# Kernel optimization log

Measured on AMD Instinct MI355X. Metric: run time of the kernel, lower is better.

## Reference

```python
import jax, jax.numpy as jnp
import numpy as np

IN_F, OUT_F, NUM_GRIDS, BATCH = 2048, 2048, 8, 4096


def setup_inputs() -> dict:
    key = jax.random.key(0)
    ks = jax.random.split(key, 5)
    x = jax.random.normal(ks[0], (BATCH, IN_F), dtype=jnp.float32)
    # kaiming_uniform_(a=sqrt(5)) on Linear weight -> U(-b, b), b = 1/sqrt(in_features)
    bound = 1.0 / np.sqrt(IN_F)
    base_w = jax.random.uniform(ks[1], (OUT_F, IN_F), dtype=jnp.float32, minval=-bound, maxval=bound)
    base_b = jnp.zeros((OUT_F,), dtype=jnp.float32)
    spline_weight = 0.1 * jax.random.normal(ks[2], (OUT_F, IN_F, NUM_GRIDS), dtype=jnp.float32)
    grid = jnp.linspace(-2.0, 2.0, NUM_GRIDS, dtype=jnp.float32)
    adaptive_gate = jnp.ones((OUT_F,), dtype=jnp.float32)
    feature_importance = jnp.ones((IN_F,), dtype=jnp.float32)
    return {"x": x, "base_w": base_w, "base_b": base_b,
            "spline_weight": spline_weight, "grid": grid,
            "adaptive_gate": adaptive_gate, "feature_importance": feature_importance}


def reference(x, base_w, base_b, spline_weight, grid, adaptive_gate, feature_importance):
    # feature gating
    x_weighted = x * jax.nn.sigmoid(feature_importance)[None, :]          # [b, i]
    # base path: Linear
    base_output = x_weighted @ base_w.T + base_b                          # [b, o]
    # spline path: RBF basis over grid
    x_norm = jnp.tanh(x_weighted)                                         # [b, i]
    basis = jnp.exp(-((x_norm[:, :, None] - grid[None, None, :]) ** 2) * 2.0)  # [b, i, g]
    # F.normalize(p=1, dim=-1): divide by L1 norm clamped to eps
    denom = jnp.maximum(jnp.sum(jnp.abs(basis), axis=-1, keepdims=True), 1e-12)
    basis = basis / denom
    spline_output = jnp.einsum('big,oig->bo', basis, spline_weight)       # [b, o]
    gate = jax.nn.sigmoid(adaptive_gate)[None, :]                         # [1, o]
    return gate * spline_output + (1.0 - gate) * base_output
```

## Files before the change

### kernel.cpp

```cpp
#include <hip/hip_runtime.h>
#include <hip/hip_bf16.h>

#define IN_F   2048
#define OUT_F  2048
#define NG     8
#define BATCH  4096
#define KDIM   (IN_F * (NG + 1))
#define BK     64
#define NT     (KDIM / BK)
#define BM     256
#define BN     128
#define ASZ    (BM * BK * 2)
#define BSZ    (BN * BK * 2)
#define BUFSZ  (ASZ + BSZ)

typedef short bf16x8 __attribute__((ext_vector_type(8)));
typedef float f32x4  __attribute__((ext_vector_type(4)));
typedef __attribute__((address_space(3))) unsigned char       lds_u8;
typedef const __attribute__((address_space(1))) unsigned char glb_u8;

__device__ __forceinline__ float sigmoidf_(float v) {
    return 1.0f / (1.0f + __expf(-v));
}

__device__ __forceinline__ unsigned short f2bf(float f) {
    unsigned int u = __builtin_bit_cast(unsigned int, f);
    u = (u + 0x7fffu + ((u >> 16) & 1u)) >> 16;
    return (unsigned short)u;
}

__global__ __launch_bounds__(256) void act_kernel(
    const float* __restrict__ x, const float* __restrict__ fi,
    const float* __restrict__ gr, unsigned short* __restrict__ Abf)
{
    const int base = blockIdx.x * 1024;
    const int tid  = threadIdx.x;
    const int b    = base >> 11;
    const float4 g0 = *(const float4*)gr;
    const float4 g1 = *(const float4*)(gr + 4);
    unsigned short* rowp = Abf + (size_t)b * KDIM;

#pragma unroll
    for (int e = 0; e < 4; ++e) {
        const int idx = base + tid + e * 256;
        const int i   = idx & (IN_F - 1);
        const float s  = sigmoidf_(fi[i]);
        const float xw = x[idx] * s;
        const float ex = __expf(2.0f * xw);
        const float xn = (ex - 1.0f) / (ex + 1.0f);

        float ev[NG];
        float d;
        d = xn - g0.x; ev[0] = __expf(-2.0f * d * d);
        d = xn - g0.y; ev[1] = __expf(-2.0f * d * d);
        d = xn - g0.z; ev[2] = __expf(-2.0f * d * d);
        d = xn - g0.w; ev[3] = __expf(-2.0f * d * d);
        d = xn - g1.x; ev[4] = __expf(-2.0f * d * d);
        d = xn - g1.y; ev[5] = __expf(-2.0f * d * d);
        d = xn - g1.z; ev[6] = __expf(-2.0f * d * d);
        d = xn - g1.w; ev[7] = __expf(-2.0f * d * d);
        float denom = ((ev[0] + ev[1]) + (ev[2] + ev[3])) +
                      ((ev[4] + ev[5]) + (ev[6] + ev[7]));
        const float rinv = 1.0f / fmaxf(denom, 1e-12f);

        union { unsigned short us[8]; int4 v; } pk;
#pragma unroll
        for (int g = 0; g < NG; ++g) pk.us[g] = f2bf(ev[g] * rinv);
        *(int4*)(rowp + i * NG) = pk.v;
        rowp[IN_F * NG + i] = f2bf(xw);
    }
}

__global__ __launch_bounds__(256) void wprep_kernel(
    const float* __restrict__ bw, const float* __restrict__ sw,
    const float* __restrict__ ag, unsigned short* __restrict__ Wbf)
{
    const int base = blockIdx.x * 1024;
    const int tid  = threadIdx.x;
    const int o    = base >> 11;
    const float gate = sigmoidf_(ag[o]);
    const float og   = 1.0f - gate;
    unsigned short* rowp = Wbf + (size_t)o * KDIM;

#pragma unroll
    for (int e = 0; e < 4; ++e) {
        const int idx = base + tid + e * 256;
        const int i   = idx & (IN_F - 1);
        const float4 s0 = *(const float4*)(sw + (size_t)idx * NG);
        const float4 s1 = *(const float4*)(sw + (size_t)idx * NG + 4);
        union { unsigned short us[8]; int4 v; } pk;
        pk.us[0] = f2bf(gate * s0.x); pk.us[1] = f2bf(gate * s0.y);
        pk.us[2] = f2bf(gate * s0.z); pk.us[3] = f2bf(gate * s0.w);
        pk.us[4] = f2bf(gate * s1.x); pk.us[5] = f2bf(gate * s1.y);
        pk.us[6] = f2bf(gate * s1.z); pk.us[7] = f2bf(gate * s1.w);
        *(int4*)(rowp + i * NG) = pk.v;
        rowp[IN_F * NG + i] = f2bf(og * bw[idx]);
    }
}

#define MFMA(d, a, b) d = __builtin_amdgcn_mfma_f32_16x16x32_bf16(a, b, d, 0, 0, 0)

#define LDA(m) (*(const bf16x8*)(lds + curBase + oA##m))
#define LDB(n) (*(const bf16x8*)(lds + curBase + oB##n))

#define GLA(j) __builtin_amdgcn_global_load_lds((glb_u8*)(aS##j + ko), \
                   (lds_u8*)(lds + stBase + aO##j), 16, 0, 0)
#define GLB(j) __builtin_amdgcn_global_load_lds((glb_u8*)(bS##j + ko), \
                   (lds_u8*)(lds + stBase + bO##j), 16, 0, 0)

__global__ __launch_bounds__(512, 2) void gemm_kernel(
    const unsigned short* __restrict__ A, const unsigned short* __restrict__ B,
    const float* __restrict__ bb, const float* __restrict__ ag,
    float* __restrict__ C)
{
    __shared__ __align__(16) unsigned char lds[3 * BUFSZ];

    const int tid = threadIdx.x;
    const int bid = blockIdx.x;
    const int swz = ((bid & 7) << 5) + (bid >> 3);
    const int bm = swz >> 4, bn = swz & 15;

    const int lane = tid & 63, wid = tid >> 6;
    const int ks = wid & 1, wn = (wid >> 1) & 1, wm = wid >> 2;
    const int fr = lane & 15, kg = lane >> 4;
    const int kq = 4 * ks + kg;

#define MKSA(j)                                                         \
    const int eA##j = tid + (j) * 512;                                  \
    const int rA_##j = eA##j >> 3, cA_##j = (eA##j & 7) ^ (rA_##j & 7); \
    const unsigned short* aS##j = A + (size_t)(bm * BM + rA_##j) * KDIM + cA_##j * 8; \
    const int aO##j = eA##j * 16;
    MKSA(0) MKSA(1) MKSA(2) MKSA(3)
#define MKSB(j)                                                         \
    const int eB##j = tid + (j) * 512;                                  \
    const int rB_##j = eB##j >> 3, cB_##j = (eB##j & 7) ^ (rB_##j & 7); \
    const unsigned short* bS##j = B + (size_t)(bn * BN + rB_##j) * KDIM + cB_##j * 8; \
    const int bO##j = ASZ + eB##j * 16;
    MKSB(0) MKSB(1)

#define MKOA(m)                                                \
    const int rAm##m = wm * 128 + (m) * 16 + fr;               \
    const int oA##m = rAm##m * 128 + ((kq ^ (rAm##m & 7)) << 4);
    MKOA(0) MKOA(1) MKOA(2) MKOA(3) MKOA(4) MKOA(5) MKOA(6) MKOA(7)
#define MKOB(n)                                                \
    const int rBn##n = wn * 64 + (n) * 16 + fr;                \
    const int oB##n = ASZ + rBn##n * 128 + ((kq ^ (rBn##n & 7)) << 4);
    MKOB(0) MKOB(1) MKOB(2) MKOB(3)

    f32x4 acc[8][4] = {};

    {
        const int stBase = 0; const long ko = 0;
        GLA(0); GLA(1); GLA(2); GLA(3); GLB(0); GLB(1);
    }
    {
        const int stBase = BUFSZ; const long ko = BK;
        GLA(0); GLA(1); GLA(2); GLA(3); GLB(0); GLB(1);
    }
    asm volatile("s_waitcnt vmcnt(6)" ::: "memory");
    __builtin_amdgcn_s_barrier();
    __builtin_amdgcn_sched_barrier(0);

    int curBase = 0;
    for (int t = 0; t < NT; ++t) {
        const int stBase = (curBase >= BUFSZ) ? (curBase - BUFSZ)
                                              : (curBase + 2 * BUFSZ);
        const bool doSt = (t + 2) < NT;
        const long ko = (long)(t + 2) * BK;

        bf16x8 vb0 = LDB(0), vb1 = LDB(1), vb2 = LDB(2), vb3 = LDB(3);
        bf16x8 va0 = LDA(0), va1 = LDA(1), va2 = LDA(2), va3 = LDA(3);
        bf16x8 va4 = LDA(4), va5 = LDA(5), va6 = LDA(6), va7 = LDA(7);
        if (doSt) { GLA(0); GLA(1); GLA(2); GLA(3); GLB(0); GLB(1); }

        __builtin_amdgcn_s_setprio(1);
        MFMA(acc[0][0], va0, vb0); MFMA(acc[0][1], va0, vb1);
        MFMA(acc[0][2], va0, vb2); MFMA(acc[0][3], va0, vb3);
        MFMA(acc[1][0], va1, vb0); MFMA(acc[1][1], va1, vb1);
        MFMA(acc[1][2], va1, vb2); MFMA(acc[1][3], va1, vb3);
        MFMA(acc[2][0], va2, vb0); MFMA(acc[2][1], va2, vb1);
        MFMA(acc[2][2], va2, vb2); MFMA(acc[2][3], va2, vb3);
        MFMA(acc[3][0], va3, vb0); MFMA(acc[3][1], va3, vb1);
        MFMA(acc[3][2], va3, vb2); MFMA(acc[3][3], va3, vb3);
        MFMA(acc[4][0], va4, vb0); MFMA(acc[4][1], va4, vb1);
        MFMA(acc[4][2], va4, vb2); MFMA(acc[4][3], va4, vb3);
        MFMA(acc[5][0], va5, vb0); MFMA(acc[5][1], va5, vb1);
        MFMA(acc[5][2], va5, vb2); MFMA(acc[5][3], va5, vb3);
        MFMA(acc[6][0], va6, vb0); MFMA(acc[6][1], va6, vb1);
        MFMA(acc[6][2], va6, vb2); MFMA(acc[6][3], va6, vb3);
        MFMA(acc[7][0], va7, vb0); MFMA(acc[7][1], va7, vb1);
        MFMA(acc[7][2], va7, vb2); MFMA(acc[7][3], va7, vb3);
        __builtin_amdgcn_s_setprio(0);

        __builtin_amdgcn_sched_barrier(0);
        if (doSt) { asm volatile("s_waitcnt vmcnt(6)" ::: "memory"); }
        else      { asm volatile("s_waitcnt vmcnt(0)" ::: "memory"); }
        __builtin_amdgcn_s_barrier();
        __builtin_amdgcn_sched_barrier(0);

        curBase = (curBase == 2 * BUFSZ) ? 0 : (curBase + BUFSZ);
    }

    const int slot = wm * 2 + wn;
    if (ks == 1) {
#pragma unroll
        for (int m = 0; m < 8; ++m)
#pragma unroll
            for (int n = 0; n < 4; ++n)
                *(f32x4*)(lds + slot * 32768 + (m * 4 + n) * 1024 + lane * 16)
                    = acc[m][n];
    }
    __syncthreads();
    if (ks == 0) {
        const int colb = bn * BN + wn * 64;
        const int rowb = bm * BM + wm * 128;
#pragma unroll
        for (int n = 0; n < 4; ++n) {
            const int col = colb + n * 16 + fr;
            const float gate = sigmoidf_(ag[col]);
            const float bias = (1.0f - gate) * bb[col];
#pragma unroll
            for (int m = 0; m < 8; ++m) {
                const f32x4 part =
                    *(const f32x4*)(lds + slot * 32768 + (m * 4 + n) * 1024 + lane * 16);
                const int r0 = rowb + m * 16 + kg * 4;
#pragma unroll
                for (int j = 0; j < 4; ++j)
                    C[(size_t)(r0 + j) * OUT_F + col] = acc[m][n][j] + part[j] + bias;
            }
        }
    }
}

extern "C" void kernel_launch(void* const* d_in, const int* in_sizes, int n_in,
                              void* d_out, int out_size, void* d_ws, size_t ws_size,
                              hipStream_t stream)
{
    const float* x  = (const float*)d_in[0];
    const float* bw = (const float*)d_in[1];
    const float* bb = (const float*)d_in[2];
    const float* sw = (const float*)d_in[3];
    const float* gr = (const float*)d_in[4];
    const float* ag = (const float*)d_in[5];
    const float* fi = (const float*)d_in[6];
    float* out = (float*)d_out;

    unsigned short* Abf = (unsigned short*)d_ws;
    unsigned short* Wbf = Abf + (size_t)BATCH * KDIM;

    const size_t need = ((size_t)BATCH + OUT_F) * KDIM * sizeof(unsigned short);
    if (ws_size < need) return;

    act_kernel<<<BATCH * IN_F / 1024, 256, 0, stream>>>(x, fi, gr, Abf);
    wprep_kernel<<<OUT_F * IN_F / 1024, 256, 0, stream>>>(bw, sw, ag, Wbf);
    gemm_kernel<<<(BATCH / BM) * (OUT_F / BN), 512, 0, stream>>>(Abf, Wbf, bb, ag, out);
}
```

Baseline: 533.8 us.

## Load GEMM B operand directly from global in MFMA-ready prepacked layout

The weight prep kernel now writes B in a per-column-tile, per-k-step prepacked layout, so each wave can load its MFMA B fragments straight from global memory into registers. The B staging through LDS is removed, leaving LDS for A only, and B fragments are prefetched one step ahead in registers. This cuts LDS traffic and LDS footprint per block. The cost is more global/L2 reads, since each wave fetches its own B fragments and the k-split wave pairs duplicate loads, plus extra registers for the prefetched B values.

Measured after the change: 571.0 us. 1.07x slower.

```diff
diff --git a/kernel.cpp b/kernel.cpp
--- a/kernel.cpp
+++ b/kernel.cpp
@@ -10,9 +10,7 @@
 #define NT     (KDIM / BK)
 #define BM     256
 #define BN     128
-#define ASZ    (BM * BK * 2)
-#define BSZ    (BN * BK * 2)
-#define BUFSZ  (ASZ + BSZ)
+#define ABUF   32768
 
 typedef short bf16x8 __attribute__((ext_vector_type(8)));
 typedef float f32x4  __attribute__((ext_vector_type(4)));
@@ -73,47 +71,51 @@
 
 __global__ __launch_bounds__(256) void wprep_kernel(
     const float* __restrict__ bw, const float* __restrict__ sw,
-    const float* __restrict__ ag, unsigned short* __restrict__ Wbf)
-{
-    const int base = blockIdx.x * 1024;
-    const int tid  = threadIdx.x;
-    const int o    = base >> 11;
-    const float gate = sigmoidf_(ag[o]);
-    const float og   = 1.0f - gate;
-    unsigned short* rowp = Wbf + (size_t)o * KDIM;
-
-#pragma unroll
-    for (int e = 0; e < 4; ++e) {
-        const int idx = base + tid + e * 256;
-        const int i   = idx & (IN_F - 1);
-        const float4 s0 = *(const float4*)(sw + (size_t)idx * NG);
-        const float4 s1 = *(const float4*)(sw + (size_t)idx * NG + 4);
+    const float* __restrict__ ag, unsigned short* __restrict__ Wpp)
+{
+    const int bn = blockIdx.x >> 7;
+    const int it = blockIdx.x & 127;
+    const int i0 = it * 16;
+    const int tid = threadIdx.x;
+    unsigned short* base = Wpp + (size_t)bn * 288 * 8192;
+
+#pragma unroll
+    for (int e = 0; e < 8; ++e) {
+        const int idx = e * 256 + tid;
+        const int o   = idx >> 4;
+        const int i   = i0 + (idx & 15);
+        const int go  = bn * 128 + o;
+        const float gate = sigmoidf_(ag[go]);
+        const float og   = 1.0f - gate;
+
+        const size_t srow = ((size_t)go * IN_F + i) * NG;
+        const float4 s0 = *(const float4*)(sw + srow);
+        const float4 s1 = *(const float4*)(sw + srow + 4);
         union { unsigned short us[8]; int4 v; } pk;
         pk.us[0] = f2bf(gate * s0.x); pk.us[1] = f2bf(gate * s0.y);
         pk.us[2] = f2bf(gate * s0.z); pk.us[3] = f2bf(gate * s0.w);
         pk.us[4] = f2bf(gate * s1.x); pk.us[5] = f2bf(gate * s1.y);
         pk.us[6] = f2bf(gate * s1.z); pk.us[7] = f2bf(gate * s1.w);
-        *(int4*)(rowp + i * NG) = pk.v;
-        rowp[IN_F * NG + i] = f2bf(og * bw[idx]);
+        *(int4*)(base + ((size_t)(i >> 3) * 8 + (i & 7)) * 1024 + o * 8) = pk.v;
+
+        base[((size_t)(256 + (i >> 6)) * 8 + ((i >> 3) & 7)) * 1024 + o * 8 + (i & 7)]
+            = f2bf(og * bw[(size_t)go * IN_F + i]);
     }
 }
 
 #define MFMA(d, a, b) d = __builtin_amdgcn_mfma_f32_16x16x32_bf16(a, b, d, 0, 0, 0)
 
 #define LDA(m) (*(const bf16x8*)(lds + curBase + oA##m))
-#define LDB(n) (*(const bf16x8*)(lds + curBase + oB##n))
 
 #define GLA(j) __builtin_amdgcn_global_load_lds((glb_u8*)(aS##j + ko), \
                    (lds_u8*)(lds + stBase + aO##j), 16, 0, 0)
-#define GLB(j) __builtin_amdgcn_global_load_lds((glb_u8*)(bS##j + ko), \
-                   (lds_u8*)(lds + stBase + bO##j), 16, 0, 0)
 
 __global__ __launch_bounds__(512, 2) void gemm_kernel(
     const unsigned short* __restrict__ A, const unsigned short* __restrict__ B,
     const float* __restrict__ bb, const float* __restrict__ ag,
     float* __restrict__ C)
 {
-    __shared__ __align__(16) unsigned char lds[3 * BUFSZ];
+    __shared__ __align__(16) unsigned char lds[131072];
 
     const int tid = threadIdx.x;
     const int bid = blockIdx.x;
@@ -131,74 +133,75 @@
     const unsigned short* aS##j = A + (size_t)(bm * BM + rA_##j) * KDIM + cA_##j * 8; \
     const int aO##j = eA##j * 16;
     MKSA(0) MKSA(1) MKSA(2) MKSA(3)
-#define MKSB(j)                                                         \
-    const int eB##j = tid + (j) * 512;                                  \
-    const int rB_##j = eB##j >> 3, cB_##j = (eB##j & 7) ^ (rB_##j & 7); \
-    const unsigned short* bS##j = B + (size_t)(bn * BN + rB_##j) * KDIM + cB_##j * 8; \
-    const int bO##j = ASZ + eB##j * 16;
-    MKSB(0) MKSB(1)
 
 #define MKOA(m)                                                \
     const int rAm##m = wm * 128 + (m) * 16 + fr;               \
     const int oA##m = rAm##m * 128 + ((kq ^ (rAm##m & 7)) << 4);
     MKOA(0) MKOA(1) MKOA(2) MKOA(3) MKOA(4) MKOA(5) MKOA(6) MKOA(7)
-#define MKOB(n)                                                \
-    const int rBn##n = wn * 64 + (n) * 16 + fr;                \
-    const int oB##n = ASZ + rBn##n * 128 + ((kq ^ (rBn##n & 7)) << 4);
-    MKOB(0) MKOB(1) MKOB(2) MKOB(3)
+
+    const unsigned short* Bw = B + (size_t)bn * 288 * 8192 + kq * 1024
+                                 + (wn * 64 + fr) * 8;
+#define LDBG(t_, n_) (*(const bf16x8*)(Bw + (size_t)(t_) * 8192 + (n_) * 128))
 
     f32x4 acc[8][4] = {};
 
     {
         const int stBase = 0; const long ko = 0;
-        GLA(0); GLA(1); GLA(2); GLA(3); GLB(0); GLB(1);
+        GLA(0); GLA(1); GLA(2); GLA(3);
     }
     {
-        const int stBase = BUFSZ; const long ko = BK;
-        GLA(0); GLA(1); GLA(2); GLA(3); GLB(0); GLB(1);
-    }
-    asm volatile("s_waitcnt vmcnt(6)" ::: "memory");
+        const int stBase = ABUF; const long ko = BK;
+        GLA(0); GLA(1); GLA(2); GLA(3);
+    }
+    bf16x8 cb0 = LDBG(0, 0), cb1 = LDBG(0, 1), cb2 = LDBG(0, 2), cb3 = LDBG(0, 3);
+    asm volatile("s_waitcnt vmcnt(8)" ::: "memory");
     __builtin_amdgcn_s_barrier();
     __builtin_amdgcn_sched_barrier(0);
 
     int curBase = 0;
     for (int t = 0; t < NT; ++t) {
-        const int stBase = (curBase >= BUFSZ) ? (curBase - BUFSZ)
-                                              : (curBase + 2 * BUFSZ);
+        const int stBase = (curBase == 0) ? 2 * ABUF
+                         : (curBase == ABUF) ? 0 : ABUF;
+        const bool doB  = (t + 1) < NT;
         const bool doSt = (t + 2) < NT;
         const long ko = (long)(t + 2) * BK;
 
-        bf16x8 vb0 = LDB(0), vb1 = LDB(1), vb2 = LDB(2), vb3 = LDB(3);
+        bf16x8 nb0, nb1, nb2, nb3;
+        if (doB) { nb0 = LDBG(t + 1, 0); nb1 = LDBG(t + 1, 1);
+                   nb2 = LDBG(t + 1, 2); nb3 = LDBG(t + 1, 3); }
+        if (doSt) { GLA(0); GLA(1); GLA(2); GLA(3); }
+
         bf16x8 va0 = LDA(0), va1 = LDA(1), va2 = LDA(2), va3 = LDA(3);
         bf16x8 va4 = LDA(4), va5 = LDA(5), va6 = LDA(6), va7 = LDA(7);
-        if (doSt) { GLA(0); GLA(1); GLA(2); GLA(3); GLB(0); GLB(1); }
 
         __builtin_amdgcn_s_setprio(1);
-        MFMA(acc[0][0], va0, vb0); MFMA(acc[0][1], va0, vb1);
-        MFMA(acc[0][2], va0, vb2); MFMA(acc[0][3], va0, vb3);
-        MFMA(acc[1][0], va1, vb0); MFMA(acc[1][1], va1, vb1);
-        MFMA(acc[1][2], va1, vb2); MFMA(acc[1][3], va1, vb3);
-        MFMA(acc[2][0], va2, vb0); MFMA(acc[2][1], va2, vb1);
-        MFMA(acc[2][2], va2, vb2); MFMA(acc[2][3], va2, vb3);
-        MFMA(acc[3][0], va3, vb0); MFMA(acc[3][1], va3, vb1);
-        MFMA(acc[3][2], va3, vb2); MFMA(acc[3][3], va3, vb3);
-        MFMA(acc[4][0], va4, vb0); MFMA(acc[4][1], va4, vb1);
-        MFMA(acc[4][2], va4, vb2); MFMA(acc[4][3], va4, vb3);
-        MFMA(acc[5][0], va5, vb0); MFMA(acc[5][1], va5, vb1);
-        MFMA(acc[5][2], va5, vb2); MFMA(acc[5][3], va5, vb3);
-        MFMA(acc[6][0], va6, vb0); MFMA(acc[6][1], va6, vb1);
-        MFMA(acc[6][2], va6, vb2); MFMA(acc[6][3], va6, vb3);
-        MFMA(acc[7][0], va7, vb0); MFMA(acc[7][1], va7, vb1);
-        MFMA(acc[7][2], va7, vb2); MFMA(acc[7][3], va7, vb3);
+        MFMA(acc[0][0], va0, cb0); MFMA(acc[0][1], va0, cb1);
+        MFMA(acc[0][2], va0, cb2); MFMA(acc[0][3], va0, cb3);
+        MFMA(acc[1][0], va1, cb0); MFMA(acc[1][1], va1, cb1);
+        MFMA(acc[1][2], va1, cb2); MFMA(acc[1][3], va1, cb3);
+        MFMA(acc[2][0], va2, cb0); MFMA(acc[2][1], va2, cb1);
+        MFMA(acc[2][2], va2, cb2); MFMA(acc[2][3], va2, cb3);
+        MFMA(acc[3][0], va3, cb0); MFMA(acc[3][1], va3, cb1);
+        MFMA(acc[3][2], va3, cb2); MFMA(acc[3][3], va3, cb3);
+        MFMA(acc[4][0], va4, cb0); MFMA(acc[4][1], va4, cb1);
+        MFMA(acc[4][2], va4, cb2); MFMA(acc[4][3], va4, cb3);
+        MFMA(acc[5][0], va5, cb0); MFMA(acc[5][1], va5, cb1);
+        MFMA(acc[5][2], va5, cb2); MFMA(acc[5][3], va5, cb3);
+        MFMA(acc[6][0], va6, cb0); MFMA(acc[6][1], va6, cb1);
+        MFMA(acc[6][2], va6, cb2); MFMA(acc[6][3], va6, cb3);
+        MFMA(acc[7][0], va7, cb0); MFMA(acc[7][1], va7, cb1);
+        MFMA(acc[7][2], va7, cb2); MFMA(acc[7][3], va7, cb3);
         __builtin_amdgcn_s_setprio(0);
 
         __builtin_amdgcn_sched_barrier(0);
-        if (doSt) { asm volatile("s_waitcnt vmcnt(6)" ::: "memory"); }
-        else      { asm volatile("s_waitcnt vmcnt(0)" ::: "memory"); }
+        if (doSt)      { asm volatile("s_waitcnt vmcnt(8)" ::: "memory"); }
+        else if (doB)  { asm volatile("s_waitcnt vmcnt(4)" ::: "memory"); }
+        else           { asm volatile("s_waitcnt vmcnt(0)" ::: "memory"); }
         __builtin_amdgcn_s_barrier();
         __builtin_amdgcn_sched_barrier(0);
 
-        curBase = (curBase == 2 * BUFSZ) ? 0 : (curBase + BUFSZ);
+        if (doB) { cb0 = nb0; cb1 = nb1; cb2 = nb2; cb3 = nb3; }
+        curBase = (curBase == 2 * ABUF) ? 0 : (curBase + ABUF);
     }
 
     const int slot = wm * 2 + wn;
@@ -246,12 +249,12 @@
     float* out = (float*)d_out;
 
     unsigned short* Abf = (unsigned short*)d_ws;
-    unsigned short* Wbf = Abf + (size_t)BATCH * KDIM;
+    unsigned short* Wpp = Abf + (size_t)BATCH * KDIM;
 
     const size_t need = ((size_t)BATCH + OUT_F) * KDIM * sizeof(unsigned short);
     if (ws_size < need) return;
 
     act_kernel<<<BATCH * IN_F / 1024, 256, 0, stream>>>(x, fi, gr, Abf);
-    wprep_kernel<<<OUT_F * IN_F / 1024, 256, 0, stream>>>(bw, sw, ag, Wbf);
-    gemm_kernel<<<(BATCH / BM) * (OUT_F / BN), 512, 0, stream>>>(Abf, Wbf, bb, ag, out);
-}
+    wprep_kernel<<<16 * 128, 256, 0, stream>>>(bw, sw, ag, Wpp);
+    gemm_kernel<<<(BATCH / BM) * (OUT_F / BN), 512, 0, stream>>>(Abf, Wpp, bb, ag, out);
+}
```

## Shrink GEMM tile to 128x128 with double buffering for higher occupancy

Applied to the files above, without the earlier changes.

Halves the M tile from 256 to 128 rows, cuts the LDS ring from three stages to two (64 KB total), and raises launch bounds to four blocks per CU. The block swizzle is remapped to a 32x16 grid of tiles and the prefetch depth drops from two tiles ahead to one, with a full vmcnt(0) wait every iteration. The aim is more resident waves to hide latency, at the cost of lower operand reuse per tile (more global traffic) and less prefetch slack per wave.

Result: slower. 577.9 us (+8.3%).

```diff
diff --git a/kernel.cpp b/kernel.cpp
--- a/kernel.cpp
+++ b/kernel.cpp
@@ -8,11 +8,9 @@
 #define KDIM   (IN_F * (NG + 1))
 #define BK     64
 #define NT     (KDIM / BK)
-#define BM     256
+#define BM     128
 #define BN     128
-#define ASZ    (BM * BK * 2)
-#define BSZ    (BN * BK * 2)
-#define BUFSZ  (ASZ + BSZ)
+#define TBUF   32768
 
 typedef short bf16x8 __attribute__((ext_vector_type(8)));
 typedef float f32x4  __attribute__((ext_vector_type(4)));
@@ -108,17 +106,17 @@
 #define GLB(j) __builtin_amdgcn_global_load_lds((glb_u8*)(bS##j + ko), \
                    (lds_u8*)(lds + stBase + bO##j), 16, 0, 0)
 
-__global__ __launch_bounds__(512, 2) void gemm_kernel(
+__global__ __launch_bounds__(512, 4) void gemm_kernel(
     const unsigned short* __restrict__ A, const unsigned short* __restrict__ B,
     const float* __restrict__ bb, const float* __restrict__ ag,
     float* __restrict__ C)
 {
-    __shared__ __align__(16) unsigned char lds[3 * BUFSZ];
+    __shared__ __align__(16) unsigned char lds[2 * TBUF];
 
     const int tid = threadIdx.x;
     const int bid = blockIdx.x;
-    const int swz = ((bid & 7) << 5) + (bid >> 3);
-    const int bm = swz >> 4, bn = swz & 15;
+    const int swz = ((bid & 7) << 6) + (bid >> 3);
+    const int bn = swz >> 5, bm = swz & 31;
 
     const int lane = tid & 63, wid = tid >> 6;
     const int ks = wid & 1, wn = (wid >> 1) & 1, wm = wid >> 2;
@@ -130,48 +128,42 @@
     const int rA_##j = eA##j >> 3, cA_##j = (eA##j & 7) ^ (rA_##j & 7); \
     const unsigned short* aS##j = A + (size_t)(bm * BM + rA_##j) * KDIM + cA_##j * 8; \
     const int aO##j = eA##j * 16;
-    MKSA(0) MKSA(1) MKSA(2) MKSA(3)
+    MKSA(0) MKSA(1)
 #define MKSB(j)                                                         \
     const int eB##j = tid + (j) * 512;                                  \
     const int rB_##j = eB##j >> 3, cB_##j = (eB##j & 7) ^ (rB_##j & 7); \
     const unsigned short* bS##j = B + (size_t)(bn * BN + rB_##j) * KDIM + cB_##j * 8; \
-    const int bO##j = ASZ + eB##j * 16;
+    const int bO##j = 16384 + eB##j * 16;
     MKSB(0) MKSB(1)
 
 #define MKOA(m)                                                \
-    const int rAm##m = wm * 128 + (m) * 16 + fr;               \
+    const int rAm##m = wm * 64 + (m) * 16 + fr;                \
     const int oA##m = rAm##m * 128 + ((kq ^ (rAm##m & 7)) << 4);
-    MKOA(0) MKOA(1) MKOA(2) MKOA(3) MKOA(4) MKOA(5) MKOA(6) MKOA(7)
+    MKOA(0) MKOA(1) MKOA(2) MKOA(3)
 #define MKOB(n)                                                \
     const int rBn##n = wn * 64 + (n) * 16 + fr;                \
-    const int oB##n = ASZ + rBn##n * 128 + ((kq ^ (rBn##n & 7)) << 4);
+    const int oB##n = 16384 + rBn##n * 128 + ((kq ^ (rBn##n & 7)) << 4);
     MKOB(0) MKOB(1) MKOB(2) MKOB(3)
 
-    f32x4 acc[8][4] = {};
+    f32x4 acc[4][4] = {};
 
     {
         const int stBase = 0; const long ko = 0;
-        GLA(0); GLA(1); GLA(2); GLA(3); GLB(0); GLB(1);
-    }
-    {
-        const int stBase = BUFSZ; const long ko = BK;
-        GLA(0); GLA(1); GLA(2); GLA(3); GLB(0); GLB(1);
-    }
-    asm volatile("s_waitcnt vmcnt(6)" ::: "memory");
+        GLA(0); GLA(1); GLB(0); GLB(1);
+    }
+    asm volatile("s_waitcnt vmcnt(0)" ::: "memory");
     __builtin_amdgcn_s_barrier();
     __builtin_amdgcn_sched_barrier(0);
 
     int curBase = 0;
     for (int t = 0; t < NT; ++t) {
-        const int stBase = (curBase >= BUFSZ) ? (curBase - BUFSZ)
-                                              : (curBase + 2 * BUFSZ);
-        const bool doSt = (t + 2) < NT;
-        const long ko = (long)(t + 2) * BK;
+        const int stBase = curBase ^ TBUF;
+        const bool doSt = (t + 1) < NT;
+        const long ko = (long)(t + 1) * BK;
 
         bf16x8 vb0 = LDB(0), vb1 = LDB(1), vb2 = LDB(2), vb3 = LDB(3);
         bf16x8 va0 = LDA(0), va1 = LDA(1), va2 = LDA(2), va3 = LDA(3);
-        bf16x8 va4 = LDA(4), va5 = LDA(5), va6 = LDA(6), va7 = LDA(7);
-        if (doSt) { GLA(0); GLA(1); GLA(2); GLA(3); GLB(0); GLB(1); }
+        if (doSt) { GLA(0); GLA(1); GLB(0); GLB(1); }
 
         __builtin_amdgcn_s_setprio(1);
         MFMA(acc[0][0], va0, vb0); MFMA(acc[0][1], va0, vb1);
@@ -182,47 +174,38 @@
         MFMA(acc[2][2], va2, vb2); MFMA(acc[2][3], va2, vb3);
         MFMA(acc[3][0], va3, vb0); MFMA(acc[3][1], va3, vb1);
         MFMA(acc[3][2], va3, vb2); MFMA(acc[3][3], va3, vb3);
-        MFMA(acc[4][0], va4, vb0); MFMA(acc[4][1], va4, vb1);
-        MFMA(acc[4][2], va4, vb2); MFMA(acc[4][3], va4, vb3);
-        MFMA(acc[5][0], va5, vb0); MFMA(acc[5][1], va5, vb1);
-        MFMA(acc[5][2], va5, vb2); MFMA(acc[5][3], va5, vb3);
-        MFMA(acc[6][0], va6, vb0); MFMA(acc[6][1], va6, vb1);
-        MFMA(acc[6][2], va6, vb2); MFMA(acc[6][3], va6, vb3);
-        MFMA(acc[7][0], va7, vb0); MFMA(acc[7][1], va7, vb1);
-        MFMA(acc[7][2], va7, vb2); MFMA(acc[7][3], va7, vb3);
         __builtin_amdgcn_s_setprio(0);
 
         __builtin_amdgcn_sched_barrier(0);
-        if (doSt) { asm volatile("s_waitcnt vmcnt(6)" ::: "memory"); }
-        else      { asm volatile("s_waitcnt vmcnt(0)" ::: "memory"); }
+        asm volatile("s_waitcnt vmcnt(0)" ::: "memory");
         __builtin_amdgcn_s_barrier();
         __builtin_amdgcn_sched_barrier(0);
 
-        curBase = (curBase == 2 * BUFSZ) ? 0 : (curBase + BUFSZ);
+        curBase ^= TBUF;
     }
 
     const int slot = wm * 2 + wn;
     if (ks == 1) {
 #pragma unroll
-        for (int m = 0; m < 8; ++m)
+        for (int m = 0; m < 4; ++m)
 #pragma unroll
             for (int n = 0; n < 4; ++n)
-                *(f32x4*)(lds + slot * 32768 + (m * 4 + n) * 1024 + lane * 16)
+                *(f32x4*)(lds + slot * 16384 + (m * 4 + n) * 1024 + lane * 16)
                     = acc[m][n];
     }
     __syncthreads();
     if (ks == 0) {
         const int colb = bn * BN + wn * 64;
-        const int rowb = bm * BM + wm * 128;
+        const int rowb = bm * BM + wm * 64;
 #pragma unroll
         for (int n = 0; n < 4; ++n) {
             const int col = colb + n * 16 + fr;
             const float gate = sigmoidf_(ag[col]);
             const float bias = (1.0f - gate) * bb[col];
 #pragma unroll
-            for (int m = 0; m < 8; ++m) {
+            for (int m = 0; m < 4; ++m) {
                 const f32x4 part =
-                    *(const f32x4*)(lds + slot * 32768 + (m * 4 + n) * 1024 + lane * 16);
+                    *(const f32x4*)(lds + slot * 16384 + (m * 4 + n) * 1024 + lane * 16);
                 const int r0 = rowb + m * 16 + kg * 4;
 #pragma unroll
                 for (int j = 0; j < 4; ++j)
```
